# Kernel tuning notes

Measured on AMD Instinct MI355X. Metric: run time of the kernel, lower is better.

The kernel has to match this reference:

```python
import jax, jax.numpy as jnp
import numpy as np

N_CONV = 3
FEAT = 128
N_RBF = 20
CUTOFF = 5.0
EPS = 1e-15
N_NODES = 10000
N_EDGES = 160000


def setup_inputs() -> dict:
    key = jax.random.key(0)
    ks = jax.random.split(key, 8)
    N, E = N_NODES, N_EDGES
    cg_xyz = jax.random.normal(ks[0], (N, 3), jnp.float32) * 2.0
    # Directed, self-loop-free edge list (both i<j and i>j present, so the
    # original make_directed() is a no-op on this data).
    src = jax.random.randint(ks[1], (E,), 0, N)
    off = jax.random.randint(ks[2], (E,), 1, N)
    CG_nbr_list = jnp.stack([src, (src + off) % N], axis=1)
    cg_s = jax.random.normal(ks[3], (N, FEAT), jnp.float32)
    s = 1.0 / np.sqrt(FEAT)
    # Per-conv-layer weights of ENMessageBlock: inv_dense = Dense(F->F, silu) + Dense(F->3F);
    # dist_embed = ExpNormalBasis(n_rbf) -> Dense(n_rbf->3F) * cosine envelope.
    W1 = jax.random.normal(ks[4], (N_CONV, FEAT, FEAT), jnp.float32) * s
    b1 = jnp.zeros((N_CONV, FEAT), jnp.float32)
    W2 = jax.random.normal(ks[5], (N_CONV, FEAT, 3 * FEAT), jnp.float32) * s
    b2 = jnp.zeros((N_CONV, 3 * FEAT), jnp.float32)
    Wr = jax.random.normal(ks[6], (N_CONV, N_RBF, 3 * FEAT), jnp.float32) / np.sqrt(N_RBF)
    br = jnp.zeros((N_CONV, 3 * FEAT), jnp.float32)
    return {"cg_xyz": cg_xyz, "CG_nbr_list": CG_nbr_list, "cg_s": cg_s,
            "W1": W1, "b1": b1, "W2": W2, "b2": b2, "Wr": Wr, "br": br}


def _expnorm_rbf(dist):
    # ExpNormalBasis: exp(-beta * (exp(-d) - mu)^2), mu in [exp(-cutoff), 1]
    mu = jnp.linspace(np.exp(-CUTOFF), 1.0, N_RBF, dtype=jnp.float32)
    beta = np.float32((2.0 / N_RBF * (1.0 - np.exp(-CUTOFF))) ** -2)
    return jnp.exp(-beta * (jnp.exp(-dist)[:, None] - mu) ** 2)  # (E, n_rbf)


def _cos_envelope(dist):
    return jnp.where(dist < CUTOFF, 0.5 * (jnp.cos(jnp.pi * dist / CUTOFF) + 1.0), 0.0)


def reference(cg_xyz, CG_nbr_list, cg_s, W1, b1, W2, b2, Wr, br):
    N = cg_s.shape[0]
    i, j = CG_nbr_list[:, 0], CG_nbr_list[:, 1]
    r_ij = cg_xyz[j] - cg_xyz[i]                      # (E, 3)
    dist = jnp.sqrt((r_ij ** 2 + EPS).sum(-1))        # (E,)
    unit = r_ij / dist[:, None]                        # (E, 3)
    rbf = _expnorm_rbf(dist)                           # (E, n_rbf) edge-invariant across layers
    env = _cos_envelope(dist)[:, None]                 # (E, 1)

    s_i = cg_s                                         # (N, F)
    v_i = jnp.zeros((N, FEAT, 3), cg_s.dtype)          # (N, F, 3)
    for l in range(N_CONV):
        phi = jax.nn.silu(s_i @ W1[l] + b1[l]) @ W2[l] + b2[l]   # (N, 3F)
        w_s = (rbf @ Wr[l] + br[l]) * env                         # (E, 3F)
        prod = phi[j] * w_s                                       # (E, 3F) gather + gate
        ds = prod[:, :FEAT]                                       # scalar message
        gate_v = prod[:, FEAT:2 * FEAT]                           # gates v_j
        gate_u = prod[:, 2 * FEAT:]                               # gates unit vector
        dv_ij = gate_u[:, :, None] * unit[:, None, :] + gate_v[:, :, None] * v_i[j]  # (E, F, 3)
        s_i = s_i + jax.ops.segment_sum(ds, i, num_segments=N)
        v_i = v_i + jax.ops.segment_sum(dv_ij, i, num_segments=N)
    return s_i, v_i
```

## Files before the change

kernel.cpp:

```cpp
#include <hip/hip_runtime.h>
#include <hip/hip_bf16.h>

#define NRBF 20
#define KAUG 24

typedef __attribute__((ext_vector_type(8))) short short8;
typedef __attribute__((ext_vector_type(4))) float float4v;
typedef __attribute__((ext_vector_type(2))) _Float16 half2v;
typedef unsigned short ushort_t;

__device__ __forceinline__ float bf2f(ushort_t u) {
    return __uint_as_float(((unsigned)u) << 16);
}
__device__ __forceinline__ ushort_t f2bf(float f) {
    unsigned u = __float_as_uint(f);
    u += 0x7FFF + ((u >> 16) & 1);
    return (ushort_t)(u >> 16);
}
__device__ __forceinline__ float ldin(const void* p, size_t idx, int isbf) {
    return isbf ? bf2f(((const ushort_t*)p)[idx]) : ((const float*)p)[idx];
}
__device__ __forceinline__ void stout(void* p, size_t idx, float v, int isbf) {
    if (isbf) ((ushort_t*)p)[idx] = f2bf(v);
    else      ((float*)p)[idx] = v;
}
__device__ __forceinline__ float dot2(half2v a, half2v b, float c) {
#if __has_builtin(__builtin_amdgcn_fdot2)
    return __builtin_amdgcn_fdot2(a, b, c, false);
#else
    return c + (float)a.x * (float)b.x + (float)a.y * (float)b.y;
#endif
}

__global__ void detect_kernel(const void* __restrict__ xyz, int* __restrict__ flag,
                              int* __restrict__ deg, int N) {
    int idx = blockIdx.x * blockDim.x + threadIdx.x;
    if (idx < N) deg[idx] = 0;
    if (blockIdx.x == 0 && threadIdx.x < 64) {
        const ushort_t* u = (const ushort_t*)xyz;
        unsigned e0 = (u[2 * threadIdx.x] >> 7) & 0xFF;
        unsigned long long bad = __ballot(e0 >= 0x90);
        if (threadIdx.x == 0) *flag = (__popcll(bad) > 2) ? 0 : 1;
    }
}

__global__ void prelude_kernel(const void* __restrict__ xyz, const int* __restrict__ nbr,
                               const void* __restrict__ cg_s,
                               const void* __restrict__ W1, const void* __restrict__ W2,
                               const void* __restrict__ Wr, const void* __restrict__ br,
                               float* __restrict__ s_acc, ushort_t* __restrict__ s_hi,
                               ushort_t* __restrict__ s_lo, int* __restrict__ deg,
                               ushort_t* __restrict__ B1hi, ushort_t* __restrict__ B1lo,
                               ushort_t* __restrict__ B2hi, ushort_t* __restrict__ B2lo,
                               _Float16* __restrict__ WrT,
                               int N128, int E, const int* __restrict__ flagp) {
    int isbf = *flagp;
    int idx = blockIdx.x * blockDim.x + threadIdx.x;
    if (idx < E) {
        int i = nbr[2 * idx], j = nbr[2 * idx + 1];
        float dx = ldin(xyz, 3 * j,     isbf) - ldin(xyz, 3 * i,     isbf);
        float dy = ldin(xyz, 3 * j + 1, isbf) - ldin(xyz, 3 * i + 1, isbf);
        float dz = ldin(xyz, 3 * j + 2, isbf) - ldin(xyz, 3 * i + 2, isbf);
        float dist = sqrtf(dx * dx + dy * dy + dz * dz + 3e-15f);
        if (dist < 5.0f) atomicAdd(&deg[i], 1);
    }
    if (idx < N128) {
        float v = ldin(cg_s, idx, isbf);
        s_acc[idx] = v;
        ushort_t hi = f2bf(v);
        s_hi[idx] = hi;
        s_lo[idx] = f2bf(v - bf2f(hi));
    }
    const int NW1 = 3 * 4 * 8 * 64;
    const int NW2 = 3 * 4 * 24 * 64;
    const int NWT = 3 * 384;
    if (idx < NW1) {
        int lane = idx & 63;
        int t = idx >> 6;
        int nt = t % 8; t /= 8;
        int ks = t % 4; int l = t / 4;
        int n = lane & 15, quad = lane >> 4;
        int col = nt * 16 + n;
        size_t base = (size_t)l * 128 * 128;
        size_t fo = (size_t)idx * 8;
        #pragma unroll
        for (int j = 0; j < 8; j++) {
            int k = ks * 32 + quad * 8 + j;
            float v = ldin(W1, base + (size_t)k * 128 + col, isbf);
            ushort_t hi = f2bf(v);
            B1hi[fo + j] = hi;
            B1lo[fo + j] = f2bf(v - bf2f(hi));
        }
    } else if (idx < NW1 + NW2) {
        int i2 = idx - NW1;
        int lane = i2 & 63;
        int t = i2 >> 6;
        int nt = t % 24; t /= 24;
        int ks = t % 4; int l = t / 4;
        int n = lane & 15, quad = lane >> 4;
        int col = nt * 16 + n;
        size_t base = (size_t)l * 128 * 384;
        size_t fo = (size_t)i2 * 8;
        #pragma unroll
        for (int j = 0; j < 8; j++) {
            int k = ks * 32 + quad * 8 + j;
            float v = ldin(W2, base + (size_t)k * 384 + col, isbf);
            ushort_t hi = f2bf(v);
            B2hi[fo + j] = hi;
            B2lo[fo + j] = f2bf(v - bf2f(hi));
        }
    } else if (idx < NW1 + NW2 + NWT) {
        int i2 = idx - NW1 - NW2;
        int l = i2 / 384, col = i2 % 384;
        _Float16* wt = WrT + ((size_t)l * 384 + col) * KAUG;
        #pragma unroll
        for (int k = 0; k < KAUG; k++) {
            float v = 0.f;
            if (k < NRBF) v = ldin(Wr, ((size_t)l * NRBF + k) * 384 + col, isbf);
            else if (k == NRBF) v = ldin(br, (size_t)l * 384 + col, isbf);
            wt[k] = (_Float16)v;
        }
    }
}

__global__ void scan_kernel(int* __restrict__ deg, int* __restrict__ rowptr, int N) {
    __shared__ int part[256];
    int t = threadIdx.x;
    int chunk = (N + 255) / 256;
    int lo = t * chunk, hi = min(lo + chunk, N);
    int s = 0;
    for (int i = lo; i < hi; i++) s += deg[i];
    part[t] = s;
    __syncthreads();
    for (int off = 1; off < 256; off <<= 1) {
        int v = (t >= off) ? part[t - off] : 0;
        __syncthreads();
        if (t >= off) part[t] += v;
        __syncthreads();
    }
    int base = (t == 0) ? 0 : part[t - 1];
    for (int i = lo; i < hi; i++) {
        rowptr[i] = base;
        int d = deg[i];
        deg[i] = base;
        base += d;
    }
    if (t == 0) rowptr[N] = part[255];
}

__global__ void pack_kernel(const void* __restrict__ xyz, const int* __restrict__ nbr,
                            int* __restrict__ cursor, int* __restrict__ jlist,
                            float4* __restrict__ upos, _Float16* __restrict__ rbfh,
                            int E, const int* __restrict__ flagp) {
    int isbf = *flagp;
    int e = blockIdx.x * blockDim.x + threadIdx.x;
    if (e >= E) return;
    int i = nbr[2 * e], j = nbr[2 * e + 1];
    float dx = ldin(xyz, 3 * j,     isbf) - ldin(xyz, 3 * i,     isbf);
    float dy = ldin(xyz, 3 * j + 1, isbf) - ldin(xyz, 3 * i + 1, isbf);
    float dz = ldin(xyz, 3 * j + 2, isbf) - ldin(xyz, 3 * i + 2, isbf);
    float dist = sqrtf(dx * dx + dy * dy + dz * dz + 3e-15f);
    if (!(dist < 5.0f)) return;
    constexpr float PI = 3.14159265358979323846f;
    float ev = 0.5f * (cosf(PI * dist * 0.2f) + 1.0f);
    int pos = atomicAdd(&cursor[i], 1);
    jlist[pos] = j;
    float inv = 1.0f / dist;
    upos[pos] = make_float4(dx * inv, dy * inv, dz * inv, ev);
    constexpr double EM5 = 0.006737946999085467;
    constexpr float MU0 = (float)EM5;
    constexpr float DMU = (float)((1.0 - EM5) / 19.0);
    constexpr float BETA = (float)(1.0 / ((0.1 * (1.0 - EM5)) * (0.1 * (1.0 - EM5))));
    float ed = expf(-dist);
    _Float16* rp = rbfh + (size_t)pos * KAUG;
    #pragma unroll
    for (int k = 0; k < NRBF; k++) {
        float dmu = ed - (MU0 + k * DMU);
        rp[k] = (_Float16)(ev * expf(-BETA * dmu * dmu));
    }
    rp[NRBF] = (_Float16)ev;
    #pragma unroll
    for (int k = NRBF + 1; k < KAUG; k++) rp[k] = (_Float16)0.f;
}

template <int ACT, int OUTMODE, int NTILES>
__global__ __launch_bounds__(256) void mfma_gemm(
    const ushort_t* __restrict__ Ahi, const ushort_t* __restrict__ Alo,
    const ushort_t* __restrict__ Bhi, const ushort_t* __restrict__ Blo,
    const void* __restrict__ bias, size_t biasoff,
    ushort_t* __restrict__ out_hi, ushort_t* __restrict__ out_lo,
    int M, const int* __restrict__ flagp) {
    constexpr int Ncols = NTILES * 16;
    int isbf = *flagp;
    int nt = blockIdx.x % NTILES;
    int bx = blockIdx.x / NTILES;
    int tid = threadIdx.x;
    int wave = tid >> 6, lane = tid & 63;
    int m = lane & 15, quad = lane >> 4;
    int brow = bx * 64 + wave * 16;
    int row = brow + m;
    float4v acc = {};
    short8 zero8 = {};
    #pragma unroll
    for (int ks = 0; ks < 4; ks++) {
        short8 ah = zero8, al = zero8;
        if (row < M) {
            size_t ao = (size_t)row * 128 + ks * 32 + quad * 8;
            ah = *reinterpret_cast<const short8*>(Ahi + ao);
            al = *reinterpret_cast<const short8*>(Alo + ao);
        }
        size_t fo = (((size_t)ks * NTILES + nt) * 64 + lane) * 8;
        short8 bh = *reinterpret_cast<const short8*>(Bhi + fo);
        acc = __builtin_amdgcn_mfma_f32_16x16x32_bf16(ah, bh, acc, 0, 0, 0);
        acc = __builtin_amdgcn_mfma_f32_16x16x32_bf16(al, bh, acc, 0, 0, 0);
        if (!isbf) {
            short8 bl = *reinterpret_cast<const short8*>(Blo + fo);
            acc = __builtin_amdgcn_mfma_f32_16x16x32_bf16(ah, bl, acc, 0, 0, 0);
        }
    }
    int col = nt * 16 + m;
    float bv = ldin(bias, biasoff + col, isbf);
    #pragma unroll
    for (int r = 0; r < 4; r++) {
        int orow = brow + quad * 4 + r;
        if (orow >= M) continue;
        float x = acc[r] + bv;
        if (ACT) x = x / (1.0f + expf(-x));
        size_t oo = (size_t)orow * Ncols + col;
        ushort_t h = f2bf(x);
        out_hi[oo] = h;
        if (OUTMODE == 0) out_lo[oo] = f2bf(x - bf2f(h));
    }
}

template <int L0, int LAST>
__global__ __launch_bounds__(128, 8) void node_kernel(
    const int* __restrict__ rowptr, const int* __restrict__ jlist,
    const float4* __restrict__ upos, const _Float16* __restrict__ rbfh,
    const _Float16* __restrict__ WrT,
    const ushort_t* __restrict__ phi,
    const float* __restrict__ v_old, const ushort_t* __restrict__ vh_old,
    float* __restrict__ s_acc, ushort_t* __restrict__ s_hi, ushort_t* __restrict__ s_lo,
    float* __restrict__ v_new, ushort_t* __restrict__ vh_new,
    void* __restrict__ out, int N, const int* __restrict__ flagp) {
    int isbf = *flagp;
    int tt = threadIdx.x;
    int node = blockIdx.x;

    half2v wc0[11], wc1[11], wc2[11];
    {
        const half2v* w0p = (const half2v*)(WrT + (size_t)tt * KAUG);
        const half2v* w1p = (const half2v*)(WrT + (size_t)(tt + 128) * KAUG);
        const half2v* w2p = (const half2v*)(WrT + (size_t)(tt + 256) * KAUG);
        #pragma unroll
        for (int k = 0; k < 11; k++) {
            wc0[k] = w0p[k]; wc1[k] = w1p[k]; wc2[k] = w2p[k];
        }
    }
    int start = __builtin_amdgcn_readfirstlane(rowptr[node]);
    int end   = __builtin_amdgcn_readfirstlane(rowptr[node + 1]);

    float dsv = 0.f, ax = 0.f, ay = 0.f, az = 0.f;
    for (int k = start; k < end; k++) {
        int j = __builtin_amdgcn_readfirstlane(jlist[k]);
        float4 u4 = upos[k];
        const half2v* rp = (const half2v*)(rbfh + (size_t)k * KAUG);
        float w0 = 0.f, w1 = 0.f, w2 = 0.f;
        #pragma unroll
        for (int r = 0; r < 11; r++) {
            half2v rv = rp[r];
            w0 = dot2(rv, wc0[r], w0);
            w1 = dot2(rv, wc1[r], w1);
            w2 = dot2(rv, wc2[r], w2);
        }
        size_t jb = (size_t)j * 384;
        dsv += bf2f(phi[jb + tt]) * w0;
        float gv = bf2f(phi[jb + 128 + tt]) * w1;
        float gu = bf2f(phi[jb + 256 + tt]) * w2;
        if (L0) {
            ax += gu * u4.x; ay += gu * u4.y; az += gu * u4.z;
        } else {
            const ushort_t* vj = &vh_old[jb + (size_t)tt * 3];
            ax += gu * u4.x + gv * bf2f(vj[0]);
            ay += gu * u4.y + gv * bf2f(vj[1]);
            az += gu * u4.z + gv * bf2f(vj[2]);
        }
    }
    size_t so = (size_t)node * 128 + tt;
    float snew = s_acc[so] + dsv;
    size_t ib = (size_t)node * 384 + (size_t)tt * 3;
    float vx = L0 ? ax : v_old[ib]     + ax;
    float vy = L0 ? ay : v_old[ib + 1] + ay;
    float vz = L0 ? az : v_old[ib + 2] + az;
    if (LAST) {
        stout(out, so, snew, isbf);
        size_t ob = (size_t)N * 128 + ib;
        stout(out, ob,     vx, isbf);
        stout(out, ob + 1, vy, isbf);
        stout(out, ob + 2, vz, isbf);
    } else {
        s_acc[so] = snew;
        ushort_t hi = f2bf(snew);
        s_hi[so] = hi;
        s_lo[so] = f2bf(snew - bf2f(hi));
        v_new[ib] = vx; v_new[ib + 1] = vy; v_new[ib + 2] = vz;
        vh_new[ib]     = f2bf(vx);
        vh_new[ib + 1] = f2bf(vy);
        vh_new[ib + 2] = f2bf(vz);
    }
}

extern "C" void kernel_launch(void* const* d_in, const int* in_sizes, int n_in,
                              void* d_out, int out_size, void* d_ws, size_t ws_size,
                              hipStream_t stream) {
    const int N = in_sizes[0] / 3;
    const int E = in_sizes[1] / 2;
    const void* xyz  = d_in[0];
    const int*  nbr  = (const int*)d_in[1];
    const void* cg_s = d_in[2];
    const void* W1   = d_in[3];
    const void* b1   = d_in[4];
    const void* W2   = d_in[5];
    const void* b2   = d_in[6];
    const void* Wr   = d_in[7];
    const void* br   = d_in[8];

    size_t off = 0;
    auto alloc = [&](size_t bytes) -> char* {
        char* p = (char*)d_ws + off;
        off = (off + bytes + 63) & ~(size_t)63;
        return p;
    };
    int*       flag   = (int*)alloc(64);
    float*     s_acc  = (float*)alloc((size_t)N * 128 * 4);
    float*     vA     = (float*)alloc((size_t)N * 384 * 4);
    float*     vB     = (float*)alloc((size_t)N * 384 * 4);
    int*       rowptr = (int*)alloc((size_t)(N + 1) * 4);
    int*       deg    = (int*)alloc((size_t)N * 4);
    int*       jlist  = (int*)alloc((size_t)E * 4);
    float4*    upos   = (float4*)alloc((size_t)(E + 16) * 16);
    _Float16*  rbfh   = (_Float16*)alloc((size_t)(E + 16) * KAUG * 2);
    _Float16*  WrT    = (_Float16*)alloc((size_t)3 * 384 * KAUG * 2);
    ushort_t*  s_hi   = (ushort_t*)alloc((size_t)N * 128 * 2);
    ushort_t*  s_lo   = (ushort_t*)alloc((size_t)N * 128 * 2);
    ushort_t*  h_hi   = (ushort_t*)alloc((size_t)N * 128 * 2);
    ushort_t*  h_lo   = (ushort_t*)alloc((size_t)N * 128 * 2);
    ushort_t*  phi    = (ushort_t*)alloc((size_t)N * 384 * 2);
    ushort_t*  vhA    = (ushort_t*)alloc((size_t)N * 384 * 2);
    ushort_t*  vhB    = (ushort_t*)alloc((size_t)N * 384 * 2);
    ushort_t*  B1hi   = (ushort_t*)alloc((size_t)3 * 4 * 8 * 64 * 8 * 2);
    ushort_t*  B1lo   = (ushort_t*)alloc((size_t)3 * 4 * 8 * 64 * 8 * 2);
    ushort_t*  B2hi   = (ushort_t*)alloc((size_t)3 * 4 * 24 * 64 * 8 * 2);
    ushort_t*  B2lo   = (ushort_t*)alloc((size_t)3 * 4 * 24 * 64 * 8 * 2);

    detect_kernel<<<(N + 255) / 256, 256, 0, stream>>>(xyz, flag, deg, N);
    const int N128 = N * 128;
    const int pg = (max(E, N128) + 255) / 256;
    prelude_kernel<<<pg, 256, 0, stream>>>(xyz, nbr, cg_s, W1, W2, Wr, br,
                                           s_acc, s_hi, s_lo, deg,
                                           B1hi, B1lo, B2hi, B2lo, WrT,
                                           N128, E, flag);
    scan_kernel<<<1, 256, 0, stream>>>(deg, rowptr, N);
    pack_kernel<<<(E + 255) / 256, 256, 0, stream>>>(xyz, nbr, deg, jlist, upos,
                                                     rbfh, E, flag);

    const int gx = (N + 63) / 64;
    for (int l = 0; l < 3; l++) {
        mfma_gemm<1, 0, 8><<<gx * 8, 256, 0, stream>>>(
            s_hi, s_lo,
            B1hi + (size_t)l * 4 * 8 * 64 * 8, B1lo + (size_t)l * 4 * 8 * 64 * 8,
            b1, (size_t)l * 128, h_hi, h_lo, N, flag);
        mfma_gemm<0, 1, 24><<<gx * 24, 256, 0, stream>>>(
            h_hi, h_lo,
            B2hi + (size_t)l * 4 * 24 * 64 * 8, B2lo + (size_t)l * 4 * 24 * 64 * 8,
            b2, (size_t)l * 384, phi, (ushort_t*)nullptr, N, flag);
        const _Float16* wrt = WrT + (size_t)l * 384 * KAUG;
        if (l == 0) {
            node_kernel<1, 0><<<N, 128, 0, stream>>>(
                rowptr, jlist, upos, rbfh, wrt, phi,
                vA, vhA, s_acc, s_hi, s_lo, vA, vhA, d_out, N, flag);
        } else if (l == 1) {
            node_kernel<0, 0><<<N, 128, 0, stream>>>(
                rowptr, jlist, upos, rbfh, wrt, phi,
                vA, vhA, s_acc, s_hi, s_lo, vB, vhB, d_out, N, flag);
        } else {
            node_kernel<0, 1><<<N, 128, 0, stream>>>(
                rowptr, jlist, upos, rbfh, wrt, phi,
                vB, vhB, s_acc, s_hi, s_lo, vB, vhB, d_out, N, flag);
        }
    }
}
```

Baseline: 327.2 us.

## Prefetch next edge's data in node kernel and widen RBF/weight loads

The node kernel's edge loop is software-pipelined: the neighbor index, unit vector, RBF row, phi gathers and v_j gathers for edge k+1 are issued before the dot products for edge k run. This hides gather latency within each block. The RBF and weight row stride is padded from 24 to 32 halves so each row loads as three 16-byte vectors instead of eleven 4-byte loads. The launch-bounds occupancy hint drops from 8 to 4 blocks to leave room for the extra prefetch registers, and the neighbor index is no longer forced scalar with readfirstlane.

```diff
diff --git a/kernel.cpp b/kernel.cpp
--- a/kernel.cpp
+++ b/kernel.cpp
@@ -2,12 +2,15 @@
 #include <hip/hip_bf16.h>
 
 #define NRBF 20
-#define KAUG 24
+#define KAUG 32
 
 typedef __attribute__((ext_vector_type(8))) short short8;
 typedef __attribute__((ext_vector_type(4))) float float4v;
 typedef __attribute__((ext_vector_type(2))) _Float16 half2v;
+typedef __attribute__((ext_vector_type(8))) _Float16 half8v;
 typedef unsigned short ushort_t;
+
+union H8 { half8v v8; half2v v2[4]; };
 
 __device__ __forceinline__ float bf2f(ushort_t u) {
     return __uint_as_float(((unsigned)u) << 16);
@@ -180,7 +183,7 @@
     }
     rp[NRBF] = (_Float16)ev;
     #pragma unroll
-    for (int k = NRBF + 1; k < KAUG; k++) rp[k] = (_Float16)0.f;
+    for (int k = NRBF + 1; k < 24; k++) rp[k] = (_Float16)0.f;
 }
 
 template <int ACT, int OUTMODE, int NTILES>
@@ -234,7 +237,7 @@
 }
 
 template <int L0, int LAST>
-__global__ __launch_bounds__(128, 8) void node_kernel(
+__global__ __launch_bounds__(128, 4) void node_kernel(
     const int* __restrict__ rowptr, const int* __restrict__ jlist,
     const float4* __restrict__ upos, const _Float16* __restrict__ rbfh,
     const _Float16* __restrict__ WrT,
@@ -247,43 +250,72 @@
     int tt = threadIdx.x;
     int node = blockIdx.x;
 
-    half2v wc0[11], wc1[11], wc2[11];
+    H8 wcA[3], wcB[3], wcC[3];
     {
-        const half2v* w0p = (const half2v*)(WrT + (size_t)tt * KAUG);
-        const half2v* w1p = (const half2v*)(WrT + (size_t)(tt + 128) * KAUG);
-        const half2v* w2p = (const half2v*)(WrT + (size_t)(tt + 256) * KAUG);
+        const half8v* w0p = (const half8v*)(WrT + (size_t)tt * KAUG);
+        const half8v* w1p = (const half8v*)(WrT + (size_t)(tt + 128) * KAUG);
+        const half8v* w2p = (const half8v*)(WrT + (size_t)(tt + 256) * KAUG);
         #pragma unroll
-        for (int k = 0; k < 11; k++) {
-            wc0[k] = w0p[k]; wc1[k] = w1p[k]; wc2[k] = w2p[k];
+        for (int q = 0; q < 3; q++) {
+            wcA[q].v8 = w0p[q]; wcB[q].v8 = w1p[q]; wcC[q].v8 = w2p[q];
         }
     }
     int start = __builtin_amdgcn_readfirstlane(rowptr[node]);
     int end   = __builtin_amdgcn_readfirstlane(rowptr[node + 1]);
 
     float dsv = 0.f, ax = 0.f, ay = 0.f, az = 0.f;
-    for (int k = start; k < end; k++) {
-        int j = __builtin_amdgcn_readfirstlane(jlist[k]);
-        float4 u4 = upos[k];
-        const half2v* rp = (const half2v*)(rbfh + (size_t)k * KAUG);
-        float w0 = 0.f, w1 = 0.f, w2 = 0.f;
-        #pragma unroll
-        for (int r = 0; r < 11; r++) {
-            half2v rv = rp[r];
-            w0 = dot2(rv, wc0[r], w0);
-            w1 = dot2(rv, wc1[r], w1);
-            w2 = dot2(rv, wc2[r], w2);
-        }
-        size_t jb = (size_t)j * 384;
-        dsv += bf2f(phi[jb + tt]) * w0;
-        float gv = bf2f(phi[jb + 128 + tt]) * w1;
-        float gu = bf2f(phi[jb + 256 + tt]) * w2;
-        if (L0) {
-            ax += gu * u4.x; ay += gu * u4.y; az += gu * u4.z;
-        } else {
+    if (start < end) {
+        int j_c = jlist[start];
+        float4 u_c = upos[start];
+        const half8v* rp = (const half8v*)(rbfh + (size_t)start * KAUG);
+        H8 r0, r1, r2;
+        r0.v8 = rp[0]; r1.v8 = rp[1]; r2.v8 = rp[2];
+        size_t jb = (size_t)j_c * 384;
+        ushort_t p0 = phi[jb + tt], p1 = phi[jb + 128 + tt], p2 = phi[jb + 256 + tt];
+        ushort_t v0 = 0, v1 = 0, v2 = 0;
+        if (!L0) {
             const ushort_t* vj = &vh_old[jb + (size_t)tt * 3];
-            ax += gu * u4.x + gv * bf2f(vj[0]);
-            ay += gu * u4.y + gv * bf2f(vj[1]);
-            az += gu * u4.z + gv * bf2f(vj[2]);
+            v0 = vj[0]; v1 = vj[1]; v2 = vj[2];
+        }
+        for (int k = start; k < end; k++) {
+            int kn = (k + 1 < end) ? k + 1 : k;
+            int j_n = jlist[kn];
+            float4 u_n = upos[kn];
+            const half8v* rpn = (const half8v*)(rbfh + (size_t)kn * KAUG);
+            H8 n0, n1, n2;
+            n0.v8 = rpn[0]; n1.v8 = rpn[1]; n2.v8 = rpn[2];
+            size_t jbn = (size_t)j_n * 384;
+            ushort_t q0 = phi[jbn + tt], q1 = phi[jbn + 128 + tt], q2 = phi[jbn + 256 + tt];
+            ushort_t x0 = 0, x1 = 0, x2 = 0;
+            if (!L0) {
+                const ushort_t* vjn = &vh_old[jbn + (size_t)tt * 3];
+                x0 = vjn[0]; x1 = vjn[1]; x2 = vjn[2];
+            }
+            float w0 = 0.f, w1 = 0.f, w2 = 0.f;
+            #pragma unroll
+            for (int q = 0; q < 3; q++) {
+                const H8& rq = (q == 0) ? r0 : (q == 1) ? r1 : r2;
+                #pragma unroll
+                for (int p = 0; p < 4; p++) {
+                    half2v pr = rq.v2[p];
+                    w0 = dot2(pr, wcA[q].v2[p], w0);
+                    w1 = dot2(pr, wcB[q].v2[p], w1);
+                    w2 = dot2(pr, wcC[q].v2[p], w2);
+                }
+            }
+            dsv += bf2f(p0) * w0;
+            float gv = bf2f(p1) * w1;
+            float gu = bf2f(p2) * w2;
+            if (L0) {
+                ax += gu * u_c.x; ay += gu * u_c.y; az += gu * u_c.z;
+            } else {
+                ax += gu * u_c.x + gv * bf2f(v0);
+                ay += gu * u_c.y + gv * bf2f(v1);
+                az += gu * u_c.z + gv * bf2f(v2);
+            }
+            u_c = u_n; r0 = n0; r1 = n1; r2 = n2;
+            p0 = q0; p1 = q1; p2 = q2;
+            v0 = x0; v1 = x1; v2 = x2;
         }
     }
     size_t so = (size_t)node * 128 + tt;
```

Measured after the change: 339.6 us. 3.8% more time.
